# Kernel tuning notes

Hardware: AMD Instinct MI355X
Metric: run time of the kernel (lower is better)

## Reference

```python
import jax, jax.numpy as jnp
import numpy as np
from jax import lax

LEVEL = 128  # level_num

def _bn(x, g, b, m, v):
    # inference-mode BatchNorm, channel axis = 1
    sh = (1, -1) + (1,) * (x.ndim - 2)
    return (x - m.reshape(sh)) * (g.reshape(sh) * lax.rsqrt(v.reshape(sh) + 1e-5)) + b.reshape(sh)

def _leaky(a):
    return jnp.where(a > 0, a, 0.01 * a)

def _l2n(a):
    return a / jnp.maximum(jnp.linalg.norm(a, axis=1, keepdims=True), 1e-12)

def _resize_bilinear_ac(x, oh, ow):
    # bilinear, align_corners=True, NCHW
    n, c, h, w = x.shape
    ys = jnp.linspace(0.0, h - 1.0, oh)
    xs = jnp.linspace(0.0, w - 1.0, ow)
    y0 = jnp.floor(ys).astype(jnp.int32)
    x0 = jnp.floor(xs).astype(jnp.int32)
    y1 = jnp.minimum(y0 + 1, h - 1)
    x1 = jnp.minimum(x0 + 1, w - 1)
    wy = (ys - y0)[:, None]
    wx = (xs - x0)[None, :]
    Y0, Y1, X0, X1 = y0[:, None], y1[:, None], x0[None, :], x1[None, :]
    return (x[:, :, Y0, X0] * (1 - wy) * (1 - wx) + x[:, :, Y0, X1] * (1 - wy) * wx
            + x[:, :, Y1, X0] * wy * (1 - wx) + x[:, :, Y1, X1] * wy * wx)

def _forward(x, conv1_w, bn1_g, bn1_b, bn1_m, bn1_v, conv2_w, f1_w, f2_w, f2_g, f2_b, f2_m, f2_v,
             out1_w, out1_g, out1_b, out1_m, out1_v, k_w, q_w, v_w, out_w, out_g, out_b, out_m, out_v):
    # conv1: 3x3 conv + BN + LeakyReLU
    y = lax.conv_general_dilated(x, conv1_w, (1, 1), 'SAME', dimension_numbers=('NCHW', 'OIHW', 'NCHW'))
    y = _leaky(_bn(y, bn1_g, bn1_b, bn1_m, bn1_v))
    # conv2: 1x1 conv, 256->128
    x2 = jnp.einsum('nchw,oc->nohw', y, conv2_w)
    N, C, H, W = x2.shape  # C = 128
    x_ave = x2.mean(axis=(2, 3), keepdims=True)  # [N,C,1,1]
    cos = (_l2n(x_ave) * _l2n(x2)).sum(1)        # [N,H,W]
    sh, sw = H // 3, W // 3
    L = sh * sw
    # H,W divisible by 3 -> adaptive_avg_pool2d is identity
    cs = cos.reshape(N, 3, sh, 3, sw).transpose(0, 1, 3, 2, 4).reshape(N, 9, L).transpose(0, 2, 1)  # [N,L,9]
    # LBP bit packing vs center (index 4); weight 0 at index 4 (strict > gives 0 there)
    bits = (cs > cs[:, :, 4:5]).astype(x.dtype)
    wts = jnp.array([1, 2, 4, 8, 0, 16, 32, 64, 128], dtype=x.dtype)
    code = (bits * wts).sum(-1)  # [N,L]
    mn = code.min(-1, keepdims=True)
    mx = code.max(-1, keepdims=True)
    code = (code - mn) / (mx - mn)
    cmin = code.min(-1, keepdims=True)
    cmax = code.max(-1, keepdims=True)
    qlv = (2 * jnp.arange(LEVEL, dtype=x.dtype) + 1) / (2 * LEVEL) * (cmax - cmin) + cmin  # [N,LEVEL]
    inter = (qlv[:, 1] - qlv[:, 0])[:, None, None]  # [N,1,1]
    quant = 1 - jnp.abs(qlv[:, None, :] - code[:, :, None])  # [N,L,LEVEL]
    quant = jnp.where(quant > 1 - inter, quant, 0.0)
    sta = quant.sum(1)                                       # [N,LEVEL]
    sta = sta / sta.sum(-1, keepdims=True)
    sta2 = jnp.stack([qlv, sta], axis=1)                     # [N,2,LEVEL]
    h1 = _leaky(jnp.einsum('ncl,oc->nol', sta2, f1_w))       # f1: 2->64
    h2 = jax.nn.relu(_bn(jnp.einsum('ncl,oc->nol', h1, f2_w), f2_g, f2_b, f2_m, f2_v))  # f2: 64->128
    xa = jnp.broadcast_to(x_ave[:, :, 0, 0][:, :, None], (N, C, LEVEL))
    s = jnp.concatenate([h2, xa], axis=1)                    # [N,256,LEVEL]
    s = jax.nn.relu(_bn(jnp.einsum('ncl,oc->nol', s, out1_w), out1_g, out1_b, out1_m, out1_v))
    k = jnp.einsum('ncl,oc->nol', s, k_w)
    q = jnp.einsum('ncl,oc->nol', s, q_w)
    v = jnp.einsum('ncl,oc->nol', s, v_w)
    w = jax.nn.softmax(jnp.einsum('ncl,ncm->nlm', k, q), axis=-1)  # bmm(k^T, q)
    f = jnp.einsum('nlm,ncm->ncl', w, v)                            # bmm(w, v^T) then transpose
    f = jax.nn.relu(_bn(jnp.einsum('ncl,oc->nol', f, out_w), out_g, out_b, out_m, out_v))
    out = jnp.einsum('ncl,npl->ncp', f, quant).reshape(N, 256, sh, sh)  # bmm(f, quant^T)
    return _resize_bilinear_ac(out, H, W)

def setup_inputs() -> dict:
    key = jax.random.key(0)
    ks = jax.random.split(key, 16)
    f32 = jnp.float32
    def nrm(k, shape, s=0.05):
        return s * jax.random.normal(k, shape, f32)
    def bnp(k, c):
        k1, k2, k3, k4 = jax.random.split(k, 4)
        return (1.0 + 0.1 * jax.random.normal(k1, (c,), f32),
                0.1 * jax.random.normal(k2, (c,), f32),
                0.1 * jax.random.normal(k3, (c,), f32),
                jax.random.uniform(k4, (c,), f32, 0.5, 1.5))
    d = {}
    d['x'] = jax.random.normal(ks[0], (32, 512, 48, 48), f32)
    d['conv1_w'] = nrm(ks[1], (256, 512, 3, 3))
    d['bn1_g'], d['bn1_b'], d['bn1_m'], d['bn1_v'] = bnp(ks[2], 256)
    d['conv2_w'] = nrm(ks[3], (128, 256))
    d['f1_w'] = nrm(ks[4], (64, 2), 0.3)
    d['f2_w'] = nrm(ks[5], (128, 64), 0.1)
    d['f2_g'], d['f2_b'], d['f2_m'], d['f2_v'] = bnp(ks[6], 128)
    d['out1_w'] = nrm(ks[7], (256, 256))
    d['out1_g'], d['out1_b'], d['out1_m'], d['out1_v'] = bnp(ks[8], 256)
    d['k_w'] = nrm(ks[9], (256, 256))
    d['q_w'] = nrm(ks[10], (256, 256))
    d['v_w'] = nrm(ks[11], (256, 256))
    d['out_w'] = nrm(ks[12], (256, 256))
    d['out_g'], d['out_b'], d['out_m'], d['out_v'] = bnp(ks[13], 256)
    return d

def reference(x, conv1_w, bn1_g, bn1_b, bn1_m, bn1_v, conv2_w, f1_w, f2_w, f2_g, f2_b, f2_m, f2_v,
              out1_w, out1_g, out1_b, out1_m, out1_v, k_w, q_w, v_w, out_w, out_g, out_b, out_m, out_v):
    return _forward(x, conv1_w, bn1_g, bn1_b, bn1_m, bn1_v, conv2_w, f1_w, f2_w, f2_g, f2_b, f2_m, f2_v,
                    out1_w, out1_g, out1_b, out1_m, out1_v, k_w, q_w, v_w, out_w, out_g, out_b, out_m, out_v)
```

## Files before the change

### kernel.cpp

```cpp
#include <hip/hip_runtime.h>
#include <math.h>

#define N_IMG 32
#define P2304 2304
#define CIN 512
#define CMID 256
#define C2 128
#define LEV 128

typedef _Float16 half8 __attribute__((ext_vector_type(8)));
typedef float f32x16 __attribute__((ext_vector_type(16)));
typedef unsigned short u16;
typedef unsigned int u32;

__device__ __forceinline__ float wredSum(float v){
#pragma unroll
  for (int o = 32; o > 0; o >>= 1) v += __shfl_down(v, o, 64);
  return v;
}
__device__ __forceinline__ float wredMax(float v){
#pragma unroll
  for (int o = 32; o > 0; o >>= 1) v = fmaxf(v, __shfl_down(v, o, 64));
  return v;
}
// ... 35 lines not shown
__global__ void prep_w2_kernel(const float* __restrict__ w2,
                               uint4* __restrict__ Wh, uint4* __restrict__ Wl){
  int fid = blockIdx.x * 256 + threadIdx.x;
  int lam = fid & 63;
  int c32 = (fid >> 6) & 3;
  int kt  = fid >> 8;
  int co = c32 * 32 + (lam & 31);
  half8 vh, vl;
#pragma unroll
  for (int j = 0; j < 8; ++j){
    int k = kt * 16 + ((lam >> 5) << 3) + j;
    float v = w2[co * CMID + k];
    _Float16 h = (_Float16)v;
    vh[j] = h;
    vl[j] = (_Float16)((v - (float)h) * 2048.0f);
  }
  Wh[fid] = *(uint4*)&vh;
  Wl[fid] = *(uint4*)&vl;
}

__global__ void prep_bn_kernel(const float* __restrict__ g1, const float* __restrict__ b1,
                               const float* __restrict__ m1, const float* __restrict__ v1,
                               float* __restrict__ s1, float* __restrict__ t1){
  int c = threadIdx.x;
  float s = g1[c] * (1.0f / sqrtf(v1[c] + 1e-5f));
  s1[c] = s;
  t1[c] = b1[c] - m1[c] * s;
}

__global__ void prep_x_kernel(const float* __restrict__ x,
                              u16* __restrict__ xh, u16* __restrict__ xl,
                              int n0){
  __shared__ float tile[128 * 49];
  const int t = threadIdx.x;
  const int b = blockIdx.x;
  const int n_loc = b / 50;
  const int hp = b - n_loc * 50;
  const int n = n0 + n_loc;
  const int h = hp - 1;
  const bool vrow = (h >= 0) && (h < 48);
  const size_t base_n = (size_t)n_loc * 1280000;
  for (int cc = 0; cc < 4; ++cc){
    if (vrow){
      const float* src = x + (((size_t)n * 512 + cc * 128) * 48 + h) * 48;
#pragma unroll
      for (int i = 0; i < 24; ++i){
        int idx = t + 256 * i;
        int w = idx % 48;
        int c = idx / 48;
        tile[c * 49 + w] = src[(size_t)c * 2304 + w];
      }
    }
    __syncthreads();
    for (int i = 0; i < 13; ++i){
      int idx = t + 256 * i;
      if (idx < 3200){
        int ck_loc = idx / 400;
        int rem = idx - ck_loc * 400;
        int wp = rem >> 3;
        int clp = rem & 7;
        int w = wp - 1;
        int c_loc = ck_loc * 16 + clp * 2;
        float v0 = 0.f, v1 = 0.f;
        if (vrow && (unsigned)w < 48u){
          v0 = tile[c_loc * 49 + w];
          v1 = tile[(c_loc + 1) * 49 + w];
        }
        _Float16 h0 = (_Float16)v0, h1 = (_Float16)v1;
        _Float16 l0 = (_Float16)((v0 - (float)h0) * 2048.0f);
        _Float16 l1 = (_Float16)((v1 - (float)h1) * 2048.0f);
        union { _Float16 hh[2]; u32 uu; } ph, pl;
        ph.hh[0] = h0; ph.hh[1] = h1;
        pl.hh[0] = l0; pl.hh[1] = l1;
        size_t off = base_n + ((size_t)(cc * 8 + ck_loc) * 2500
                               + hp * 50 + wp) * 16 + clp * 2;
        *(u32*)(xh + off) = ph.uu;
        *(u32*)(xl + off) = pl.uu;
      }
    }
    __syncthreads();
  }
}

#define COMPUTE_M(CUR, KF)                                                    \
  {                                                                           \
    const int ct0 = (g & 1) * 2, pt0 = (g >> 1) * 2;                          \
    half8 fAh[2], fAl[2], fBh[2], fBl[2];                                     \
    _Pragma("unroll")                                                         \
    for (int a = 0; a < 2; ++a){                                              \
      fAh[a] = *(half8*)&Abuf[CUR][KF][0][(ct0 + a) * 512 + lam * 8];         \
      fAl[a] = *(half8*)&Abuf[CUR][KF][1][(ct0 + a) * 512 + lam * 8];         \
      fBh[a] = *(half8*)&Bbuf[CUR][KF][0][(pt0 + a) * 512 + lam * 8];         \
      fBl[a] = *(half8*)&Bbuf[CUR][KF][1][(pt0 + a) * 512 + lam * 8];         \
    }                                                                         \
    _Pragma("unroll")                                                         \
    for (int a = 0; a < 2; ++a)                                               \
      _Pragma("unroll")                                                       \
      for (int b = 0; b < 2; ++b){                                            \
        acc_hh[a][b] = __builtin_amdgcn_mfma_f32_32x32x16_f16(                \
            fAh[a], fBh[b], acc_hh[a][b], 0, 0, 0);                           \
        acc_x[a][b] = __builtin_amdgcn_mfma_f32_32x32x16_f16(                 \
            fAh[a], fBl[b], acc_x[a][b], 0, 0, 0);                            \
        acc_x[a][b] = __builtin_amdgcn_mfma_f32_32x32x16_f16(                 \
            fAl[a], fBh[b], acc_x[a][b], 0, 0, 0);                            \
      }                                                                       \
  }

#define WAITV8  asm volatile("s_waitcnt vmcnt(8)"  ::: "memory")
#define WAITV0  asm volatile("s_waitcnt vmcnt(0)"  ::: "memory")
#define BARSB { __builtin_amdgcn_s_barrier(); __builtin_amdgcn_sched_barrier(0); }

template<int NC>
__global__ __launch_bounds__(256, 2) void conv1_lds_kernel(
    const u16* __restrict__ xh, const u16* __restrict__ xl,
    const uint4* __restrict__ Wh, const uint4* __restrict__ Wl,
    const float* __restrict__ s1, const float* __restrict__ t1,
    u16* __restrict__ yh, u16* __restrict__ yl, int n0)
{
  __shared__ _Float16 Abuf[2][2][2][2048];
  __shared__ _Float16 Bbuf[2][2][2][2048];
  const int t = threadIdx.x;
  const int lam = t & 63;
  const int g = t >> 6;

  const int xcd = blockIdx.x & 7;
  const int rest = blockIdx.x >> 3;
  const int NPX = NC / 8;
  const int n_loc = xcd * NPX + rest / 36;
  const int inner = rest % 36;
  const int pt_blk = inner % 18;
  const int cot = inner / 18;
  const int n = n0 + n_loc;

  const int pbase = pt_blk * 128;
  const int khi = lam >> 5;
  const int pp = (g << 5) + (lam & 31);
  const int p = pbase + pp;
  const int ph = p / 48, pw = p - ph * 48;
  const u16* xh_n = xh + (size_t)n_loc * 1280000;
  const u16* xl_n = xl + (size_t)n_loc * 1280000;

  const int S = 144;

  f32x16 acc_hh[2][2], acc_x[2][2];
#pragma unroll
  for (int a = 0; a < 2; ++a)
#pragma unroll
    for (int b = 0; b < 2; ++b){
#pragma unroll
      for (int e = 0; e < 16; ++e){ acc_hh[a][b][e] = 0.f; acc_x[a][b][e] = 0.f; }
    }

#define ISSUE1(SV, BUF)                                                       \
  {                                                                           \
    int s_ = (SV);                                                            \
    int k0_ = 2 * s_;                                                         \
    _Pragma("unroll")                                                         \
    for (int kf = 0; kf < 2; ++kf){                                           \
      int fg_ = ((k0_ + kf) * 2 + cot) * 4 + g;                               \
      gll16(Wh + fg_ * 64 + lam, &Abuf[BUF][kf][0][t * 8]);                   \
      gll16(Wl + fg_ * 64 + lam, &Abuf[BUF][kf][1][t * 8]);                   \
    }                                                                         \
    int r_ = k0_ >> 5;                                          \
    int ck0_ = k0_ & 31;                         \
    int qpp_ = (ph + r_ / 3) * 50 + (pw + r_ % 3);            \
    _Pragma("unroll")                                                         \
    for (int kf = 0; kf < 2; ++kf){                                           \
      size_t o_ = ((size_t)(ck0_ + kf) * 2500 + qpp_) * 16 + (khi << 3);      \
      gll16(xh_n + o_, &Bbuf[BUF][kf][0][t * 8]);                             \
      gll16(xl_n + o_, &Bbuf[BUF][kf][1][t * 8]);                             \
    }                                                                         \
  }

  ISSUE1(0, 0);
  ISSUE1(1, 1);

  for (int s = 0; s < S - 1; ++s){
    WAITV8;
    BARSB;
    __builtin_amdgcn_s_setprio(1);
    COMPUTE_M(s & 1, 0);
    COMPUTE_M(s & 1, 1);
    __builtin_amdgcn_s_setprio(0);
    if (s + 2 < S){
      BARSB;
      ISSUE1(s + 2, s & 1);
    }
  }
  WAITV0;
  BARSB;
  __builtin_amdgcn_s_setprio(1);
  COMPUTE_M((S - 1) & 1, 0);
  COMPUTE_M((S - 1) & 1, 1);
  __builtin_amdgcn_s_setprio(0);
#undef ISSUE1

  const int cobase = cot * 128;
#pragma unroll
  for (int a = 0; a < 2; ++a){
    const int ctile = (g & 1) * 2 + a;
#pragma unroll
    for (int b = 0; b < 2; ++b){
      const int ptile = (g >> 1) * 2 + b;
      const int pg = pbase + ptile * 32 + (lam & 31);
#pragma unroll
      for (int q = 0; q < 4; ++q){
        const int co0 = cobase + ctile * 32 + 8 * q + 4 * khi;
        const int co16 = co0 >> 4, col = co0 & 15;
        union { _Float16 h[4]; uint2 u; } Uh, Ul;
#pragma unroll
        for (int i = 0; i < 4; ++i){
          const int rg = 4 * q + i;
          const int co = co0 + i;
          float val = acc_hh[a][b][rg] + acc_x[a][b][rg] * (1.0f / 2048.0f);
          val = val * s1[co] + t1[co];
          val = val > 0.f ? val : 0.01f * val;
          _Float16 h = (_Float16)val;
          Uh.h[i] = h;
          Ul.h[i] = (_Float16)((val - (float)h) * 2048.0f);
        }
        size_t off = (((size_t)n * 16 + co16) * P2304 + pg) * 16 + col;
        *(uint2*)(yh + off) = Uh.u;
        *(uint2*)(yl + off) = Ul.u;
      }
    }
  }
}

__global__ __launch_bounds__(256, 2) void conv2_lds_kernel(
    const u16* __restrict__ yh, const u16* __restrict__ yl,
    const uint4* __restrict__ Wh, const uint4* __restrict__ Wl,
    float* __restrict__ out)
{
  __shared__ _Float16 Abuf[2][2][2][2048];
  __shared__ _Float16 Bbuf[2][2][2][2048];
  const int t = threadIdx.x;
  const int lam = t & 63;
  const int g = t >> 6;

  const int pt_blk = blockIdx.x % 18;
  const int n = blockIdx.x / 18;
  const int pbase = pt_blk * 128;
  const int khi = lam >> 5;
  const int p = pbase + (g << 5) + (lam & 31);
  const u16* yh_n = yh + (size_t)n * 589824;
  const u16* yl_n = yl + (size_t)n * 589824;

  const int S = 8;

  f32x16 acc_hh[2][2], acc_x[2][2];
#pragma unroll
  for (int a = 0; a < 2; ++a)
#pragma unroll
    for (int b = 0; b < 2; ++b){
#pragma unroll
      for (int e = 0; e < 16; ++e){ acc_hh[a][b][e] = 0.f; acc_x[a][b][e] = 0.f; }
    }

#define ISSUE2(SV, BUF)                                                       \
  {                                                                           \
    int s_ = (SV);                                                            \
    int k0_ = 2 * s_;                                                         \
    _Pragma("unroll")                                                         \
    for (int kf = 0; kf < 2; ++kf){                                           \
      int fg_ = (k0_ + kf) * 4 + g;                                           \
      gll16(Wh + fg_ * 64 + lam, &Abuf[BUF][kf][0][t * 8]);                   \
      gll16(Wl + fg_ * 64 + lam, &Abuf[BUF][kf][1][t * 8]);                   \
    }                                                                         \
    _Pragma("unroll")                                                         \
    for (int kf = 0; kf < 2; ++kf){                                           \
      size_t o_ = ((size_t)(k0_ + kf) * P2304 + p) * 16 + (khi << 3);         \
      gll16(yh_n + o_, &Bbuf[BUF][kf][0][t * 8]);                             \
      gll16(yl_n + o_, &Bbuf[BUF][kf][1][t * 8]);                             \
    }                                                                         \
  }

  ISSUE2(0, 0);
  ISSUE2(1, 1);

  for (int s = 0; s < S - 1; ++s){
    WAITV8;
    BARSB;
    __builtin_amdgcn_s_setprio(1);
    COMPUTE_M(s & 1, 0);
    COMPUTE_M(s & 1, 1);
    __builtin_amdgcn_s_setprio(0);
    if (s + 2 < S){
      BARSB;
      ISSUE2(s + 2, s & 1);
    }
  }
  WAITV0;
  BARSB;
  __builtin_amdgcn_s_setprio(1);
  COMPUTE_M((S - 1) & 1, 0);
  COMPUTE_M((S - 1) & 1, 1);
  __builtin_amdgcn_s_setprio(0);
#undef ISSUE2

#pragma unroll
  for (int a = 0; a < 2; ++a){
    const int ctile = (g & 1) * 2 + a;
#pragma unroll
    for (int b = 0; b < 2; ++b){
      const int ptile = (g >> 1) * 2 + b;
      const int pg = pbase + ptile * 32 + (lam & 31);
#pragma unroll
      for (int rg = 0; rg < 16; ++rg){
        const int row = (rg & 3) + 8 * (rg >> 2) + 4 * khi;
        const int co = ctile * 32 + row;
        float val = acc_hh[a][b][rg] + acc_x[a][b][rg] * (1.0f / 2048.0f);
        out[((size_t)n * C2 + co) * P2304 + pg] = val;
      }
    }
  }
}

template<int R, int CPT, int COTN, bool BN>
__global__ __launch_bounds__(256, 2) void conv_mfma_kernel(
    const float* __restrict__ in, const uint4* __restrict__ Wh, const uint4* __restrict__ Wl,
    const float* __restrict__ s1, const float* __restrict__ t1, float* __restrict__ out)
{
  __shared__ _Float16 Abuf[2][2][2][2048];
  __shared__ _Float16 Bbuf[2][2][2][2048];
  const int t = threadIdx.x;
  const int lam = t & 63;
  const int g = t >> 6;

  int n, pt_blk, cot;
  if (COTN == 2){
    int xcd = blockIdx.x & 7;
    int rest = blockIdx.x >> 3;
    n = xcd * 4 + rest / 36;
    int inner = rest % 36;
    pt_blk = inner % 18;
    cot = inner / 18;
  } else {
    pt_blk = blockIdx.x % 18;
    cot = 0;
    n = blockIdx.x / 18;
  }
  const int pbase = pt_blk * 128;
  const int cobase = cot * 128;

  const int khi = lam >> 5;
  const int pp = (g << 5) + (lam & 31);
  const int p = pbase + pp;
  const int ph = p / 48, pw = p - ph * 48;
  const float* in_n = in + (size_t)n * CPT * P2304;

  const int S = (R * CPT) / 32;
  const int KTPT = CPT / 16;

  f32x16 acc_hh[2][2], acc_x[2][2];
#pragma unroll
  for (int a = 0; a < 2; ++a)
#pragma unroll
    for (int b = 0; b < 2; ++b){
#pragma unroll
      for (int e = 0; e < 16; ++e){ acc_hh[a][b][e] = 0.f; acc_x[a][b][e] = 0.f; }
    }

  uint4 rAh[2], rAl[2];
  float rB[16];
  bool vmask;

#define ISSUE(SV)                                                             \
  {                                                                           \
    int s_ = (SV);                                                            \
    _Pragma("unroll")                                                         \
    for (int kf = 0; kf < 2; ++kf){                                           \
      int fi = (((2 * s_ + kf) * COTN + cot) * 4 + g) * 64 + lam;             \
      rAh[kf] = Wh[fi];                                                       \
      rAl[kf] = Wl[fi];                                                       \
    }                                                                         \
    int r_ = (R == 1) ? 0 : ((2 * s_) / KTPT);                                \
    int cbase_ = ((2 * s_) % KTPT) * 16;                                      \
    int dh_ = (R == 1) ? 0 : (r_ / 3 - 1);                                    \
    int dw_ = (R == 1) ? 0 : (r_ - (r_ / 3) * 3 - 1);                         \
    int hh_ = ph + dh_, ww_ = pw + dw_;                                       \
    vmask = ((unsigned)hh_ < 48u) & ((unsigned)ww_ < 48u);                    \
    int hc_ = min(max(hh_, 0), 47), wc_ = min(max(ww_, 0), 47);               \
    const float* src_ = in_n + hc_ * 48 + wc_                                 \
                        + (size_t)(cbase_ + khi * 8) * P2304;                 \
    _Pragma("unroll")                                                         \
    for (int kf = 0; kf < 2; ++kf)                                            \
      _Pragma("unroll")                                                       \
      for (int j = 0; j < 8; ++j)                                             \
        rB[kf * 8 + j] = src_[(kf * 16 + j) * P2304];                         \
  }

#define STASH(NXT)                                                            \
  {                                                                           \
    _Pragma("unroll")                                                         \
    for (int kf = 0; kf < 2; ++kf){                                           \
      *(uint4*)&Abuf[NXT][kf][0][t * 8] = rAh[kf];                            \
      *(uint4*)&Abuf[NXT][kf][1][t * 8] = rAl[kf];                            \
      half8 vh, vl;                                                           \
      _Pragma("unroll")                                                       \
      for (int j = 0; j < 8; ++j){                                            \
        float v = vmask ? rB[kf * 8 + j] : 0.0f;                              \
        _Float16 h = (_Float16)v;                                             \
        vh[j] = h;                                                            \
        vl[j] = (_Float16)((v - (float)h) * 2048.0f);                         \
      }                                                                       \
      *(half8*)&Bbuf[NXT][kf][0][t * 8] = vh;                                 \
      *(half8*)&Bbuf[NXT][kf][1][t * 8] = vl;                                 \
    }                                                                         \
  }

  ISSUE(0);
  STASH(0);
  __syncthreads();

  for (int s = 0; s < S; ++s){
    const int cur = s & 1, nxt = cur ^ 1;
    const bool more = (s + 1 < S);
    if (more) ISSUE(s + 1);
    COMPUTE_M(cur, 0);
    if (more) STASH(nxt);
    COMPUTE_M(cur, 1);
    __syncthreads();
  }
#undef ISSUE
#undef STASH

  const int M = COTN * 128;
#pragma unroll
  for (int a = 0; a < 2; ++a){
    const int ctile = (g & 1) * 2 + a;
#pragma unroll
    for (int b = 0; b < 2; ++b){
      const int ptile = (g >> 1) * 2 + b;
      const int pg = pbase + ptile * 32 + (lam & 31);
#pragma unroll
      for (int rg = 0; rg < 16; ++rg){
        const int row = (rg & 3) + 8 * (rg >> 2) + 4 * (lam >> 5);
        const int co = cobase + ctile * 32 + row;
        float val = acc_hh[a][b][rg] + acc_x[a][b][rg] * (1.0f / 2048.0f);
        if (BN){
          val = val * s1[co] + t1[co];
          val = val > 0.f ? val : 0.01f * val;
        }
        out[((size_t)n * M + co) * P2304 + pg] = val;
      }
    }
  }
}

__global__ void xave_kernel(const float* __restrict__ x2, float* __restrict__ xave){
  __shared__ float red[4];
  int nc = blockIdx.x, t = threadIdx.x;
  const float* row = x2 + nc * P2304;
  float s = 0.f;
#pragma unroll
  for (int i = 0; i < 9; i++) s += row[t + 256 * i];
  float w = wredSum(s);
  if ((t & 63) == 0) red[t >> 6] = w;
  __syncthreads();
  if (t == 0) xave[nc] = (red[0] + red[1] + red[2] + red[3]) * (1.0f / 2304.0f);
}

__global__ void xan_kernel(const float* __restrict__ xave, float* __restrict__ xan){
  __shared__ float red[2];
  int n = blockIdx.x, t = threadIdx.x;
  float v = xave[n * 128 + t];
  float w = wredSum(v * v);
  if ((t & 63) == 0) red[t >> 6] = w;
  __syncthreads();
  float norm = fmaxf(sqrtf(red[0] + red[1]), 1e-12f);
  xan[n * 128 + t] = v / norm;
}

__global__ void cos_kernel(const float* __restrict__ x2, const float* __restrict__ xan,
                           float* __restrict__ cosb){
  int idx = blockIdx.x * 256 + threadIdx.x;
  if (idx >= N_IMG * P2304) return;
  int n = idx / P2304;
  int p = idx - n * P2304;
  const float* xp = x2 + n * C2 * P2304 + p;
  const float* an = xan + n * 128;
  float dot = 0.f, ss = 0.f;
  for (int c = 0; c < 128; c++){
    float v = xp[c * P2304];
    dot += an[c] * v;
    ss  += v * v;
  }
  cosb[idx] = dot / fmaxf(sqrtf(ss), 1e-12f);
}

__global__ void lbp_kernel(const float* __restrict__ cosb, float* __restrict__ code,
                           float* __restrict__ qlv){
  __shared__ float red[4];
  int n = blockIdx.x;
  int l = threadIdx.x;
  int ir = l >> 4, ic = l & 15;
  const float* cn = cosb + n * P2304;
  float cs4 = cn[(16 + ir) * 48 + (16 + ic)];
  const float wts[9] = {1.f, 2.f, 4.f, 8.f, 0.f, 16.f, 32.f, 64.f, 128.f};
  float codev = 0.f;
#pragma unroll
  for (int j = 0; j < 9; j++){
    int jr = j / 3, jc = j - 3 * (j / 3);
    float vv = cn[(jr * 16 + ir) * 48 + (jc * 16 + ic)];
    if (vv > cs4) codev += wts[j];
  }
  float w;
  w = wredMin(codev);
  if ((l & 63) == 0) red[l >> 6] = w;
  __syncthreads();
  float mn = fminf(fminf(red[0], red[1]), fminf(red[2], red[3]));
  __syncthreads();
  w = wredMax(codev);
  if ((l & 63) == 0) red[l >> 6] = w;
  __syncthreads();
  float mx = fmaxf(fmaxf(red[0], red[1]), fmaxf(red[2], red[3]));
  __syncthreads();
  float cd = (codev - mn) / (mx - mn);
  w = wredMin(cd);
  if ((l & 63) == 0) red[l >> 6] = w;
  __syncthreads();
  float cmin = fminf(fminf(red[0], red[1]), fminf(red[2], red[3]));
  __syncthreads();
  w = wredMax(cd);
  if ((l & 63) == 0) red[l >> 6] = w;
  __syncthreads();
  float cmax = fmaxf(fmaxf(red[0], red[1]), fmaxf(red[2], red[3]));
  code[n * 256 + l] = cd;
  if (l < 128){
    float tmp = (float)(2 * l + 1) * (1.0f / 256.0f);
    qlv[n * 128 + l] = tmp * (cmax - cmin) + cmin;
  }
}

__global__ void quant_kernel(const float* __restrict__ code, const float* __restrict__ qlv,
                             float* __restrict__ quantT){
  __shared__ float cs[256];
  __shared__ float qs[128];
  int n = blockIdx.x, t = threadIdx.x;
  cs[t] = code[n * 256 + t];
  if (t < 128) qs[t] = qlv[n * 128 + t];
  __syncthreads();
  float thr = 1.0f - (qs[1] - qs[0]);
  float* dst = quantT + n * LEV * 256;
#pragma unroll 4
  for (int i = 0; i < 128; i++){
    int v = t + 256 * i;
    int lv = v >> 8;
    int p = v & 255;
    float qq = 1.0f - fabsf(qs[lv] - cs[p]);
    dst[v] = (qq > thr) ? qq : 0.f;
  }
}

__global__ void sta_kernel(const float* __restrict__ quantT, float* __restrict__ sta){
  __shared__ float red[2];
  int n = blockIdx.x, i = threadIdx.x;
  const float* qr = quantT + (n * LEV + i) * 256;
  float s = 0.f;
  for (int p = 0; p < 256; p++) s += qr[p];
  float w = wredSum(s);
  if ((i & 63) == 0) red[i >> 6] = w;
  __syncthreads();
  float tot = red[0] + red[1];
  sta[n * 128 + i] = s / tot;
}

__global__ void h1_kernel(const float* __restrict__ f1w, const float* __restrict__ qlv,
                          const float* __restrict__ sta, float* __restrict__ h1){
  int idx = blockIdx.x * 256 + threadIdx.x;
  if (idx >= N_IMG * 64 * 128) return;
  int l = idx & 127;
  int n = idx >> 13;
  int o = (idx >> 7) & 63;
  float a = f1w[o * 2] * qlv[n * 128 + l] + f1w[o * 2 + 1] * sta[n * 128 + l];
  h1[idx] = a > 0.f ? a : 0.01f * a;
}

__global__ void gemm_w_kernel(const float* __restrict__ Wm, const float* __restrict__ B,
                              float* __restrict__ Cout, int Cdim, int O, int total, int mode,
                              const float* __restrict__ g, const float* __restrict__ bb,
                              const float* __restrict__ mm, const float* __restrict__ vv){
  int idx = blockIdx.x * 256 + threadIdx.x;
  if (idx >= total) return;
  int per_n = (O >> 2) << 7;
  int n = idx / per_n;
  int rem = idx - n * per_n;
  int o0 = (rem >> 7) << 2;
  int l = rem & 127;
  const float* Bn = B + (n * Cdim) * 128 + l;
  const float* w0 = Wm + (o0 + 0) * Cdim;
  const float* w1 = Wm + (o0 + 1) * Cdim;
  const float* w2 = Wm + (o0 + 2) * Cdim;
  const float* w3 = Wm + (o0 + 3) * Cdim;
  float a0 = 0, a1 = 0, a2 = 0, a3 = 0;
  for (int c = 0; c < Cdim; c++){
    float bv = Bn[c * 128];
    a0 += w0[c] * bv; a1 += w1[c] * bv; a2 += w2[c] * bv; a3 += w3[c] * bv;
  }
  float av[4] = {a0, a1, a2, a3};
#pragma unroll
  for (int j = 0; j < 4; j++){
    int o = o0 + j;
    float val = av[j];
    if (mode == 1){
      float s = g[o] * (1.0f / sqrtf(vv[o] + 1e-5f));
      val = (val - mm[o]) * s + bb[o];
      val = fmaxf(val, 0.f);
    }
    Cout[(n * O + o) * 128 + l] = val;
  }
}

__global__ void concat_kernel(const float* __restrict__ h2, const float* __restrict__ xave,
                              float* __restrict__ s){
  int idx = blockIdx.x * 256 + threadIdx.x;
  if (idx >= N_IMG * 256 * 128) return;
  int l = idx & 127;
  int c = (idx >> 7) & 255;
  int n = idx >> 15;
  s[idx] = (c < 128) ? h2[(n * 128 + c) * 128 + l] : xave[n * 128 + (c - 128)];
}

__global__ void attn_sc_kernel(const float* __restrict__ k, const float* __restrict__ q,
                               float* __restrict__ sc){
  int idx = blockIdx.x * 256 + threadIdx.x;
  if (idx >= N_IMG * 32 * 128) return;
  int m = idx & 127;
  int l0 = ((idx >> 7) & 31) << 2;
  int n = idx >> 12;
  const float* kn = k + n * 256 * 128;
  const float* qn = q + n * 256 * 128 + m;
  float a0 = 0, a1 = 0, a2 = 0, a3 = 0;
  for (int c = 0; c < 256; c++){
    float qv = qn[c * 128];
    const float* kr = kn + c * 128 + l0;
    a0 += kr[0] * qv; a1 += kr[1] * qv; a2 += kr[2] * qv; a3 += kr[3] * qv;
  }
  float* dst = sc + (n * 128 + l0) * 128 + m;
  dst[0] = a0; dst[128] = a1; dst[256] = a2; dst[384] = a3;
}

__global__ void softmax_kernel(float* __restrict__ sc){
  __shared__ float red[2];
  int row = blockIdx.x;
  int t = threadIdx.x;
  float v = sc[row * 128 + t];
  float w = wredMax(v);
  if ((t & 63) == 0) red[t >> 6] = w;
  __syncthreads();
  float mx = fmaxf(red[0], red[1]);
  float e = expf(v - mx);
  float s = wredSum(e);
  __syncthreads();
  if ((t & 63) == 0) red[t >> 6] = s;
  __syncthreads();
  sc[row * 128 + t] = e / (red[0] + red[1]);
}

__global__ void transpose_sc_kernel(const float* __restrict__ sc, float* __restrict__ scT){
  int idx = blockIdx.x * 256 + threadIdx.x;
  if (idx >= N_IMG * 128 * 128) return;
  int l = idx & 127;
  int m = (idx >> 7) & 127;
  int n = idx >> 14;
  scT[idx] = sc[(n * 128 + l) * 128 + m];
}

__global__ void attn_f_kernel(const float* __restrict__ vb, const float* __restrict__ scT,
                              float* __restrict__ f){
  int idx = blockIdx.x * 256 + threadIdx.x;
  if (idx >= N_IMG * 64 * 128) return;
  int l = idx & 127;
  int c0 = ((idx >> 7) & 63) << 2;
  int n = idx >> 13;
  const float* vn = vb + (n * 256 + c0) * 128;
  const float* sn = scT + n * 128 * 128 + l;
  float a0 = 0, a1 = 0, a2 = 0, a3 = 0;
  for (int m = 0; m < 128; m++){
    float sv = sn[m * 128];
    a0 += vn[m] * sv; a1 += vn[128 + m] * sv; a2 += vn[256 + m] * sv; a3 += vn[384 + m] * sv;
  }
  float* dst = f + (n * 256 + c0) * 128 + l;
  dst[0] = a0; dst[128] = a1; dst[256] = a2; dst[384] = a3;
}

__global__ void final_kernel(const float* __restrict__ g, const float* __restrict__ quantT,
                             float* __restrict__ outs){
  int idx = blockIdx.x * 256 + threadIdx.x;
  if (idx >= N_IMG * 64 * 256) return;
  int p = idx & 255;
  int c0 = ((idx >> 8) & 63) << 2;
  int n = idx >> 14;
  const float* gn = g + (n * 256 + c0) * 128;
// ... 10 lines not shown
__global__ void resize_kernel(const float* __restrict__ outs, float* __restrict__ dout){
  int idx = blockIdx.x * 256 + threadIdx.x;
  if (idx >= N_IMG * 256 * P2304) return;
  int ow = idx % 48;
  int tmp = idx / 48;
  int oh = tmp % 48;
  int nc = tmp / 48;
  const float* src = outs + nc * 256;
  float fy = oh * (15.0f / 47.0f);
  float fx = ow * (15.0f / 47.0f);
  int y0 = (int)fy;
  int x0 = (int)fx;
  int y1 = min(y0 + 1, 15);
  int x1 = min(x0 + 1, 15);
  float wy = fy - (float)y0;
  float wx = fx - (float)x0;
  float v00 = src[y0 * 16 + x0], v01 = src[y0 * 16 + x1];
  float v10 = src[y1 * 16 + x0], v11 = src[y1 * 16 + x1];
  dout[idx] = v00 * (1.f - wy) * (1.f - wx) + v01 * (1.f - wy) * wx
            + v10 * wy * (1.f - wx) + v11 * wy * wx;
}

extern "C" void kernel_launch(void* const* d_in, const int* in_sizes, int n_in,
                              void* d_out, int out_size, void* d_ws, size_t ws_size,
                              hipStream_t stream)
{
  const float* x       = (const float*)d_in[0];
  const float* conv1_w = (const float*)d_in[1];
  const float* bn1_g   = (const float*)d_in[2];
  const float* bn1_b   = (const float*)d_in[3];
  const float* bn1_m   = (const float*)d_in[4];
  const float* bn1_v   = (const float*)d_in[5];
  const float* conv2_w = (const float*)d_in[6];
  const float* f1_w    = (const float*)d_in[7];
  const float* f2_w    = (const float*)d_in[8];
  const float* f2_g    = (const float*)d_in[9];
  const float* f2_b    = (const float*)d_in[10];
  const float* f2_m    = (const float*)d_in[11];
  const float* f2_v    = (const float*)d_in[12];
  const float* out1_w  = (const float*)d_in[13];
  const float* out1_g  = (const float*)d_in[14];
  const float* out1_b  = (const float*)d_in[15];
  const float* out1_m  = (const float*)d_in[16];
  const float* out1_v  = (const float*)d_in[17];
  const float* k_w     = (const float*)d_in[18];
  const float* q_w     = (const float*)d_in[19];
  const float* v_w     = (const float*)d_in[20];
  const float* out_w   = (const float*)d_in[21];
  const float* out_g   = (const float*)d_in[22];
  const float* out_b   = (const float*)d_in[23];
  const float* out_m   = (const float*)d_in[24];
  const float* out_v   = (const float*)d_in[25];

  float* ws = (float*)d_ws;
  float* dout = (float*)d_out;

  float* w_y   = ws;
  float* w_x2  = ws + 18874368;
  float* w_W1h = ws + 28311552;
  float* w_W1l = ws + 28901376;
  float* w_W2h = ws + 29491200;
  float* w_W2l = ws + 29507584;
  float* w_s1  = ws + 29523968;
  float* w_t1  = ws + 29524224;
  float* w_xave = w_y + 0;
  float* w_xan  = w_y + 4096;
  float* w_cos  = w_y + 8192;
  float* w_code = w_y + 81920;
  float* w_qlv  = w_y + 90112;
  float* w_sta  = w_y + 94208;
  float* w_quant= w_y + 98304;
  float* w_h1   = w_y + 1146880;
  float* w_h2   = w_y + 1409024;
  float* w_s    = w_y + 1933312;
  float* w_k    = w_y + 2981888;
  float* w_q    = w_y + 4030464;
  float* w_v    = w_y + 5079040;
  float* w_sc   = w_y + 6127616;
  float* w_scT  = w_y + 6651904;
  float* w_f    = w_y + 7176192;
  float* w_g    = w_y + 8224768;
  float* w_outs = w_y + 9273344;
  float* w_s2   = w_y + 11370496;

  prep_w1_kernel<<<576, 256, 0, stream>>>(conv1_w, (uint4*)w_W1h, (uint4*)w_W1l);
  prep_w2_kernel<<<16, 256, 0, stream>>>(conv2_w, (uint4*)w_W2h, (uint4*)w_W2l);
  prep_bn_kernel<<<1, 256, 0, stream>>>(bn1_g, bn1_b, bn1_m, bn1_v, w_s1, w_t1);

  const size_t BASE_F = 29524480;
  const size_t XPI_F  = 640000;
  const size_t ws_f = ws_size / 4;
  int NCc = 0;
  if (ws_f >= BASE_F + 2 * 32 * XPI_F)      NCc = 32;
  else if (ws_f >= BASE_F + 2 * 16 * XPI_F) NCc = 16;

  if (NCc > 0){
    u16* w_xh = (u16*)(ws + BASE_F);
    u16* w_xl = w_xh + (size_t)NCc * 1280000;
    u16* w_yh = (u16*)w_y;
    u16* w_yl = (u16*)(w_y + 9437184);
    const int nchunk = N_IMG / NCc;
    for (int c = 0; c < nchunk; ++c){
      int n0 = c * NCc;
      prep_x_kernel<<<NCc * 50, 256, 0, stream>>>(x, w_xh, w_xl, n0);
      if (NCc == 32)
        conv1_lds_kernel<32><<<1152, 256, 0, stream>>>(
            w_xh, w_xl, (const uint4*)w_W1h, (const uint4*)w_W1l, w_s1, w_t1,
            w_yh, w_yl, n0);
      else
        conv1_lds_kernel<16><<<576, 256, 0, stream>>>(
            w_xh, w_xl, (const uint4*)w_W1h, (const uint4*)w_W1l, w_s1, w_t1,
            w_yh, w_yl, n0);
    }
    conv2_lds_kernel<<<576, 256, 0, stream>>>(
        w_yh, w_yl, (const uint4*)w_W2h, (const uint4*)w_W2l, w_x2);
  } else {
    conv_mfma_kernel<9, 512, 2, true><<<1152, 256, 0, stream>>>(
        x, (const uint4*)w_W1h, (const uint4*)w_W1l, w_s1, w_t1, w_y);
    conv_mfma_kernel<1, 256, 1, false><<<576, 256, 0, stream>>>(
        w_y, (const uint4*)w_W2h, (const uint4*)w_W2l, w_s1, w_t1, w_x2);
  }

  xave_kernel<<<4096, 256, 0, stream>>>(w_x2, w_xave);
  xan_kernel<<<32, 128, 0, stream>>>(w_xave, w_xan);
  cos_kernel<<<288, 256, 0, stream>>>(w_x2, w_xan, w_cos);
  lbp_kernel<<<32, 256, 0, stream>>>(w_cos, w_code, w_qlv);
  quant_kernel<<<32, 256, 0, stream>>>(w_code, w_qlv, w_quant);
  sta_kernel<<<32, 128, 0, stream>>>(w_quant, w_sta);
  h1_kernel<<<1024, 256, 0, stream>>>(f1_w, w_qlv, w_sta, w_h1);
  gemm_w_kernel<<<512, 256, 0, stream>>>(f2_w, w_h1, w_h2, 64, 128, N_IMG * 32 * 128, 1,
                                         f2_g, f2_b, f2_m, f2_v);
  concat_kernel<<<4096, 256, 0, stream>>>(w_h2, w_xave, w_s);
  gemm_w_kernel<<<1024, 256, 0, stream>>>(out1_w, w_s, w_s2, 256, 256, N_IMG * 64 * 128, 1,
                                          out1_g, out1_b, out1_m, out1_v);
  gemm_w_kernel<<<1024, 256, 0, stream>>>(k_w, w_s2, w_k, 256, 256, N_IMG * 64 * 128, 0,
                                          nullptr, nullptr, nullptr, nullptr);
  gemm_w_kernel<<<1024, 256, 0, stream>>>(q_w, w_s2, w_q, 256, 256, N_IMG * 64 * 128, 0,
                                          nullptr, nullptr, nullptr, nullptr);
  gemm_w_kernel<<<1024, 256, 0, stream>>>(v_w, w_s2, w_v, 256, 256, N_IMG * 64 * 128, 0,
                                          nullptr, nullptr, nullptr, nullptr);
  attn_sc_kernel<<<512, 256, 0, stream>>>(w_k, w_q, w_sc);
  softmax_kernel<<<4096, 128, 0, stream>>>(w_sc);
  transpose_sc_kernel<<<2048, 256, 0, stream>>>(w_sc, w_scT);
  attn_f_kernel<<<1024, 256, 0, stream>>>(w_v, w_scT, w_f);
  gemm_w_kernel<<<1024, 256, 0, stream>>>(out_w, w_f, w_g, 256, 256, N_IMG * 64 * 128, 1,
                                          out_g, out_b, out_m, out_v);
  final_kernel<<<2048, 256, 0, stream>>>(w_g, w_quant, w_outs);
  resize_kernel<<<73728, 256, 0, stream>>>(w_outs, dout);
}
```

Baseline: 1.624 ms.

## Deepen conv pipelines to 4 stages, split sta reduction, fuse k/q/v GEMMs

The conv1 and conv2 LDS kernels move from double-buffered two-k-fragment stages to a four-buffer ring with one k-fragment per stage and three loads in flight. This drops the second barrier per iteration and is meant to hide global-load latency better. The sta reduction is split into a wide row-sum kernel plus a small normalize kernel to raise parallelism. The three k/q/v weight GEMMs are merged into one launch. The trade-off is more barriers per unit of work, since stages are now half as large, plus one extra launch for sta.

```diff
diff --git a/kernel.cpp b/kernel.cpp
--- a/kernel.cpp
+++ b/kernel.cpp
@@ -141,7 +141,214 @@
   }
 }
 
-#define COMPUTE_M(CUR, KF)                                                    \
+#define COMPUTE_R(CUR)                                                        \
+  {                                                                           \
+    const int ct0 = (g & 1) * 2, pt0 = (g >> 1) * 2;                          \
+    half8 fAh[2], fAl[2], fBh[2], fBl[2];                                     \
+    _Pragma("unroll")                                                         \
+    for (int a = 0; a < 2; ++a){                                              \
+      fAh[a] = *(half8*)&Abuf[CUR][0][(ct0 + a) * 512 + lam * 8];             \
+      fAl[a] = *(half8*)&Abuf[CUR][1][(ct0 + a) * 512 + lam * 8];             \
+      fBh[a] = *(half8*)&Bbuf[CUR][0][(pt0 + a) * 512 + lam * 8];             \
+      fBl[a] = *(half8*)&Bbuf[CUR][1][(pt0 + a) * 512 + lam * 8];             \
+    }                                                                         \
+    _Pragma("unroll")                                                         \
+    for (int a = 0; a < 2; ++a)                                               \
+      _Pragma("unroll")                                                       \
+      for (int b = 0; b < 2; ++b){                                            \
+        acc_hh[a][b] = __builtin_amdgcn_mfma_f32_32x32x16_f16(                \
+            fAh[a], fBh[b], acc_hh[a][b], 0, 0, 0);                           \
+        acc_x[a][b] = __builtin_amdgcn_mfma_f32_32x32x16_f16(                 \
+            fAh[a], fBl[b], acc_x[a][b], 0, 0, 0);                            \
+        acc_x[a][b] = __builtin_amdgcn_mfma_f32_32x32x16_f16(                 \
+            fAl[a], fBh[b], acc_x[a][b], 0, 0, 0);                            \
+      }                                                                       \
+  }
+
+#define WAITV8  asm volatile("s_waitcnt vmcnt(8)"  ::: "memory")
+#define WAITV4  asm volatile("s_waitcnt vmcnt(4)"  ::: "memory")
+#define WAITV0  asm volatile("s_waitcnt vmcnt(0)"  ::: "memory")
+#define BARSB { __builtin_amdgcn_s_barrier(); __builtin_amdgcn_sched_barrier(0); }
+
+template<int NC>
+__global__ __launch_bounds__(256, 2) void conv1_lds_kernel(
+    const u16* __restrict__ xh, const u16* __restrict__ xl,
+    const uint4* __restrict__ Wh, const uint4* __restrict__ Wl,
+    const float* __restrict__ s1, const float* __restrict__ t1,
+    u16* __restrict__ yh, u16* __restrict__ yl, int n0)
+{
+  __shared__ _Float16 Abuf[4][2][2048];
+  __shared__ _Float16 Bbuf[4][2][2048];
+  const int t = threadIdx.x;
+  const int lam = t & 63;
+  const int g = t >> 6;
+
+  const int xcd = blockIdx.x & 7;
+  const int rest = blockIdx.x >> 3;
+  const int NPX = NC / 8;
+  const int n_loc = xcd * NPX + rest / 36;
+  const int inner = rest % 36;
+  const int pt_blk = inner % 18;
+  const int cot = inner / 18;
+  const int n = n0 + n_loc;
+
+  const int pbase = pt_blk * 128;
+  const int khi = lam >> 5;
+  const int pp = (g << 5) + (lam & 31);
+  const int p = pbase + pp;
+  const int ph = p / 48, pw = p - ph * 48;
+  const u16* xh_n = xh + (size_t)n_loc * 1280000;
+  const u16* xl_n = xl + (size_t)n_loc * 1280000;
+
+  const int S = 288;
+
+  f32x16 acc_hh[2][2], acc_x[2][2];
+#pragma unroll
+  for (int a = 0; a < 2; ++a)
+#pragma unroll
+    for (int b = 0; b < 2; ++b){
+#pragma unroll
+      for (int e = 0; e < 16; ++e){ acc_hh[a][b][e] = 0.f; acc_x[a][b][e] = 0.f; }
+    }
+
+#define ISSUE1(SV, BUF)                                                       \
+  {                                                                           \
+    int s_ = (SV);                                                            \
+    int fg_ = (s_ * 2 + cot) * 4 + g;                                         \
+    gll16(Wh + fg_ * 64 + lam, &Abuf[BUF][0][t * 8]);                         \
+    gll16(Wl + fg_ * 64 + lam, &Abuf[BUF][1][t * 8]);                         \
+    int r_ = s_ >> 5;                                           \
+    int ck_ = s_ & 31;                                       \
+    int qpp_ = (ph + r_ / 3) * 50 + (pw + r_ % 3);            \
+    size_t o_ = ((size_t)ck_ * 2500 + qpp_) * 16 + (khi << 3);                \
+    gll16(xh_n + o_, &Bbuf[BUF][0][t * 8]);                                   \
+    gll16(xl_n + o_, &Bbuf[BUF][1][t * 8]);                                   \
+  }
+
+  ISSUE1(0, 0);
+  ISSUE1(1, 1);
+  ISSUE1(2, 2);
+
+  for (int s = 0; s < S; ++s){
+    if (s < S - 2)      { WAITV8; }
+    else if (s == S - 2){ WAITV4; }
+    else                { WAITV0; }
+    BARSB;
+    __builtin_amdgcn_s_setprio(1);
+    COMPUTE_R(s & 3);
+    __builtin_amdgcn_s_setprio(0);
+    if (s + 3 < S) ISSUE1(s + 3, (s + 3) & 3);
+  }
+#undef ISSUE1
+
+  const int cobase = cot * 128;
+#pragma unroll
+  for (int a = 0; a < 2; ++a){
+    const int ctile = (g & 1) * 2 + a;
+#pragma unroll
+    for (int b = 0; b < 2; ++b){
+      const int ptile = (g >> 1) * 2 + b;
+      const int pg = pbase + ptile * 32 + (lam & 31);
+#pragma unroll
+      for (int q = 0; q < 4; ++q){
+        const int co0 = cobase + ctile * 32 + 8 * q + 4 * khi;
+        const int co16 = co0 >> 4, col = co0 & 15;
+        union { _Float16 h[4]; uint2 u; } Uh, Ul;
+#pragma unroll
+        for (int i = 0; i < 4; ++i){
+          const int rg = 4 * q + i;
+          const int co = co0 + i;
+          float val = acc_hh[a][b][rg] + acc_x[a][b][rg] * (1.0f / 2048.0f);
+          val = val * s1[co] + t1[co];
+          val = val > 0.f ? val : 0.01f * val;
+          _Float16 h = (_Float16)val;
+          Uh.h[i] = h;
+          Ul.h[i] = (_Float16)((val - (float)h) * 2048.0f);
+        }
+        size_t off = (((size_t)n * 16 + co16) * P2304 + pg) * 16 + col;
+        *(uint2*)(yh + off) = Uh.u;
+        *(uint2*)(yl + off) = Ul.u;
+      }
+    }
+  }
+}
+
+__global__ __launch_bounds__(256, 2) void conv2_lds_kernel(
+    const u16* __restrict__ yh, const u16* __restrict__ yl,
+    const uint4* __restrict__ Wh, const uint4* __restrict__ Wl,
+    float* __restrict__ out)
+{
+  __shared__ _Float16 Abuf[4][2][2048];
+  __shared__ _Float16 Bbuf[4][2][2048];
+  const int t = threadIdx.x;
+  const int lam = t & 63;
+  const int g = t >> 6;
+
+  const int pt_blk = blockIdx.x % 18;
+  const int n = blockIdx.x / 18;
+  const int pbase = pt_blk * 128;
+  const int khi = lam >> 5;
+  const int p = pbase + (g << 5) + (lam & 31);
+  const u16* yh_n = yh + (size_t)n * 589824;
+  const u16* yl_n = yl + (size_t)n * 589824;
+
+  const int S = 16;
+
+  f32x16 acc_hh[2][2], acc_x[2][2];
+#pragma unroll
+  for (int a = 0; a < 2; ++a)
+#pragma unroll
+    for (int b = 0; b < 2; ++b){
+#pragma unroll
+      for (int e = 0; e < 16; ++e){ acc_hh[a][b][e] = 0.f; acc_x[a][b][e] = 0.f; }
+    }
+
+#define ISSUE2(SV, BUF)                                                       \
+  {                                                                           \
+    int s_ = (SV);                                                            \
+    int fg_ = s_ * 4 + g;                                                     \
+    gll16(Wh + fg_ * 64 + lam, &Abuf[BUF][0][t * 8]);                         \
+    gll16(Wl + fg_ * 64 + lam, &Abuf[BUF][1][t * 8]);                         \
+    size_t o_ = ((size_t)s_ * P2304 + p) * 16 + (khi << 3);                   \
+    gll16(yh_n + o_, &Bbuf[BUF][0][t * 8]);                                   \
+    gll16(yl_n + o_, &Bbuf[BUF][1][t * 8]);                                   \
+  }
+
+  ISSUE2(0, 0);
+  ISSUE2(1, 1);
+  ISSUE2(2, 2);
+
+  for (int s = 0; s < S; ++s){
+    if (s < S - 2)      { WAITV8; }
+    else if (s == S - 2){ WAITV4; }
+    else                { WAITV0; }
+    BARSB;
+    __builtin_amdgcn_s_setprio(1);
+    COMPUTE_R(s & 3);
+    __builtin_amdgcn_s_setprio(0);
+    if (s + 3 < S) ISSUE2(s + 3, (s + 3) & 3);
+  }
+#undef ISSUE2
+
+#pragma unroll
+  for (int a = 0; a < 2; ++a){
+    const int ctile = (g & 1) * 2 + a;
+#pragma unroll
+    for (int b = 0; b < 2; ++b){
+      const int ptile = (g >> 1) * 2 + b;
+      const int pg = pbase + ptile * 32 + (lam & 31);
+#pragma unroll
+      for (int rg = 0; rg < 16; ++rg){
+        const int row = (rg & 3) + 8 * (rg >> 2) + 4 * khi;
+        const int co = ctile * 32 + row;
+        float val = acc_hh[a][b][rg] + acc_x[a][b][rg] * (1.0f / 2048.0f);
+        out[((size_t)n * C2 + co) * P2304 + pg] = val;
+      }
+    }
+  }
+}
+
+#define COMPUTE_F(CUR, KF)                                                    \
   {                                                                           \
     const int ct0 = (g & 1) * 2, pt0 = (g >> 1) * 2;                          \
     half8 fAh[2], fAl[2], fBh[2], fBl[2];                                     \
@@ -164,216 +371,6 @@
             fAl[a], fBh[b], acc_x[a][b], 0, 0, 0);                            \
       }                                                                       \
   }
-
-#define WAITV8  asm volatile("s_waitcnt vmcnt(8)"  ::: "memory")
-#define WAITV0  asm volatile("s_waitcnt vmcnt(0)"  ::: "memory")
-#define BARSB { __builtin_amdgcn_s_barrier(); __builtin_amdgcn_sched_barrier(0); }
-
-template<int NC>
-__global__ __launch_bounds__(256, 2) void conv1_lds_kernel(
-    const u16* __restrict__ xh, const u16* __restrict__ xl,
-    const uint4* __restrict__ Wh, const uint4* __restrict__ Wl,
-    const float* __restrict__ s1, const float* __restrict__ t1,
-    u16* __restrict__ yh, u16* __restrict__ yl, int n0)
-{
-  __shared__ _Float16 Abuf[2][2][2][2048];
-  __shared__ _Float16 Bbuf[2][2][2][2048];
-  const int t = threadIdx.x;
-  const int lam = t & 63;
-  const int g = t >> 6;
-
-  const int xcd = blockIdx.x & 7;
-  const int rest = blockIdx.x >> 3;
-  const int NPX = NC / 8;
-  const int n_loc = xcd * NPX + rest / 36;
-  const int inner = rest % 36;
-  const int pt_blk = inner % 18;
-  const int cot = inner / 18;
-  const int n = n0 + n_loc;
-
-  const int pbase = pt_blk * 128;
-  const int khi = lam >> 5;
-  const int pp = (g << 5) + (lam & 31);
-  const int p = pbase + pp;
-  const int ph = p / 48, pw = p - ph * 48;
-  const u16* xh_n = xh + (size_t)n_loc * 1280000;
-  const u16* xl_n = xl + (size_t)n_loc * 1280000;
-
-  const int S = 144;
-
-  f32x16 acc_hh[2][2], acc_x[2][2];
-#pragma unroll
-  for (int a = 0; a < 2; ++a)
-#pragma unroll
-    for (int b = 0; b < 2; ++b){
-#pragma unroll
-      for (int e = 0; e < 16; ++e){ acc_hh[a][b][e] = 0.f; acc_x[a][b][e] = 0.f; }
-    }
-
-#define ISSUE1(SV, BUF)                                                       \
-  {                                                                           \
-    int s_ = (SV);                                                            \
-    int k0_ = 2 * s_;                                                         \
-    _Pragma("unroll")                                                         \
-    for (int kf = 0; kf < 2; ++kf){                                           \
-      int fg_ = ((k0_ + kf) * 2 + cot) * 4 + g;                               \
-      gll16(Wh + fg_ * 64 + lam, &Abuf[BUF][kf][0][t * 8]);                   \
-      gll16(Wl + fg_ * 64 + lam, &Abuf[BUF][kf][1][t * 8]);                   \
-    }                                                                         \
-    int r_ = k0_ >> 5;                                          \
-    int ck0_ = k0_ & 31;                         \
-    int qpp_ = (ph + r_ / 3) * 50 + (pw + r_ % 3);            \
-    _Pragma("unroll")                                                         \
-    for (int kf = 0; kf < 2; ++kf){                                           \
-      size_t o_ = ((size_t)(ck0_ + kf) * 2500 + qpp_) * 16 + (khi << 3);      \
-      gll16(xh_n + o_, &Bbuf[BUF][kf][0][t * 8]);                             \
-      gll16(xl_n + o_, &Bbuf[BUF][kf][1][t * 8]);                             \
-    }                                                                         \
-  }
-
-  ISSUE1(0, 0);
-  ISSUE1(1, 1);
-
-  for (int s = 0; s < S - 1; ++s){
-    WAITV8;
-    BARSB;
-    __builtin_amdgcn_s_setprio(1);
-    COMPUTE_M(s & 1, 0);
-    COMPUTE_M(s & 1, 1);
-    __builtin_amdgcn_s_setprio(0);
-    if (s + 2 < S){
-      BARSB;
-      ISSUE1(s + 2, s & 1);
-    }
-  }
-  WAITV0;
-  BARSB;
-  __builtin_amdgcn_s_setprio(1);
-  COMPUTE_M((S - 1) & 1, 0);
-  COMPUTE_M((S - 1) & 1, 1);
-  __builtin_amdgcn_s_setprio(0);
-#undef ISSUE1
-
-  const int cobase = cot * 128;
-#pragma unroll
-  for (int a = 0; a < 2; ++a){
-    const int ctile = (g & 1) * 2 + a;
-#pragma unroll
-    for (int b = 0; b < 2; ++b){
-      const int ptile = (g >> 1) * 2 + b;
-      const int pg = pbase + ptile * 32 + (lam & 31);
-#pragma unroll
-      for (int q = 0; q < 4; ++q){
-        const int co0 = cobase + ctile * 32 + 8 * q + 4 * khi;
-        const int co16 = co0 >> 4, col = co0 & 15;
-        union { _Float16 h[4]; uint2 u; } Uh, Ul;
-#pragma unroll
-        for (int i = 0; i < 4; ++i){
-          const int rg = 4 * q + i;
-          const int co = co0 + i;
-          float val = acc_hh[a][b][rg] + acc_x[a][b][rg] * (1.0f / 2048.0f);
-          val = val * s1[co] + t1[co];
-          val = val > 0.f ? val : 0.01f * val;
-          _Float16 h = (_Float16)val;
-          Uh.h[i] = h;
-          Ul.h[i] = (_Float16)((val - (float)h) * 2048.0f);
-        }
-        size_t off = (((size_t)n * 16 + co16) * P2304 + pg) * 16 + col;
-        *(uint2*)(yh + off) = Uh.u;
-        *(uint2*)(yl + off) = Ul.u;
-      }
-    }
-  }
-}
-
-__global__ __launch_bounds__(256, 2) void conv2_lds_kernel(
-    const u16* __restrict__ yh, const u16* __restrict__ yl,
-    const uint4* __restrict__ Wh, const uint4* __restrict__ Wl,
-    float* __restrict__ out)
-{
-  __shared__ _Float16 Abuf[2][2][2][2048];
-  __shared__ _Float16 Bbuf[2][2][2][2048];
-  const int t = threadIdx.x;
-  const int lam = t & 63;
-  const int g = t >> 6;
-
-  const int pt_blk = blockIdx.x % 18;
-  const int n = blockIdx.x / 18;
-  const int pbase = pt_blk * 128;
-  const int khi = lam >> 5;
-  const int p = pbase + (g << 5) + (lam & 31);
-  const u16* yh_n = yh + (size_t)n * 589824;
-  const u16* yl_n = yl + (size_t)n * 589824;
-
-  const int S = 8;
-
-  f32x16 acc_hh[2][2], acc_x[2][2];
-#pragma unroll
-  for (int a = 0; a < 2; ++a)
-#pragma unroll
-    for (int b = 0; b < 2; ++b){
-#pragma unroll
-      for (int e = 0; e < 16; ++e){ acc_hh[a][b][e] = 0.f; acc_x[a][b][e] = 0.f; }
-    }
-
-#define ISSUE2(SV, BUF)                                                       \
-  {                                                                           \
-    int s_ = (SV);                                                            \
-    int k0_ = 2 * s_;                                                         \
-    _Pragma("unroll")                                                         \
-    for (int kf = 0; kf < 2; ++kf){                                           \
-      int fg_ = (k0_ + kf) * 4 + g;                                           \
-      gll16(Wh + fg_ * 64 + lam, &Abuf[BUF][kf][0][t * 8]);                   \
-      gll16(Wl + fg_ * 64 + lam, &Abuf[BUF][kf][1][t * 8]);                   \
-    }                                                                         \
-    _Pragma("unroll")                                                         \
-    for (int kf = 0; kf < 2; ++kf){                                           \
-      size_t o_ = ((size_t)(k0_ + kf) * P2304 + p) * 16 + (khi << 3);         \
-      gll16(yh_n + o_, &Bbuf[BUF][kf][0][t * 8]);                             \
-      gll16(yl_n + o_, &Bbuf[BUF][kf][1][t * 8]);                             \
-    }                                                                         \
-  }
-
-  ISSUE2(0, 0);
-  ISSUE2(1, 1);
-
-  for (int s = 0; s < S - 1; ++s){
-    WAITV8;
-    BARSB;
-    __builtin_amdgcn_s_setprio(1);
-    COMPUTE_M(s & 1, 0);
-    COMPUTE_M(s & 1, 1);
-    __builtin_amdgcn_s_setprio(0);
-    if (s + 2 < S){
-      BARSB;
-      ISSUE2(s + 2, s & 1);
-    }
-  }
-  WAITV0;
-  BARSB;
-  __builtin_amdgcn_s_setprio(1);
-  COMPUTE_M((S - 1) & 1, 0);
-  COMPUTE_M((S - 1) & 1, 1);
-  __builtin_amdgcn_s_setprio(0);
-#undef ISSUE2
-
-#pragma unroll
-  for (int a = 0; a < 2; ++a){
-    const int ctile = (g & 1) * 2 + a;
-#pragma unroll
-    for (int b = 0; b < 2; ++b){
-      const int ptile = (g >> 1) * 2 + b;
-      const int pg = pbase + ptile * 32 + (lam & 31);
-#pragma unroll
-      for (int rg = 0; rg < 16; ++rg){
-        const int row = (rg & 3) + 8 * (rg >> 2) + 4 * khi;
-        const int co = ctile * 32 + row;
-        float val = acc_hh[a][b][rg] + acc_x[a][b][rg] * (1.0f / 2048.0f);
-        out[((size_t)n * C2 + co) * P2304 + pg] = val;
-      }
-    }
-  }
-}
 
 template<int R, int CPT, int COTN, bool BN>
 __global__ __launch_bounds__(256, 2) void conv_mfma_kernel(
@@ -476,9 +473,9 @@
     const int cur = s & 1, nxt = cur ^ 1;
     const bool more = (s + 1 < S);
     if (more) ISSUE(s + 1);
-    COMPUTE_M(cur, 0);
+    COMPUTE_F(cur, 0);
     if (more) STASH(nxt);
-    COMPUTE_M(cur, 1);
+    COMPUTE_F(cur, 1);
     __syncthreads();
   }
 #undef ISSUE
@@ -612,17 +609,27 @@
   }
 }
 
-__global__ void sta_kernel(const float* __restrict__ quantT, float* __restrict__ sta){
+__global__ void sta_rows_kernel(const float* __restrict__ quantT, float* __restrict__ raw){
+  int b = blockIdx.x;
+  int t = threadIdx.x;
+  int n = b >> 5;
+  int row = (b & 31) * 4 + (t >> 6);
+  int lane = t & 63;
+  const float* src = quantT + ((size_t)(n * LEV + row)) * 256 + lane * 4;
+  float4 v = *(const float4*)src;
+  float s = v.x + v.y + v.z + v.w;
+  s = wredSum(s);
+  if (lane == 0) raw[n * 128 + row] = s;
+}
+
+__global__ void sta_norm_kernel(const float* __restrict__ raw, float* __restrict__ sta){
   __shared__ float red[2];
-  int n = blockIdx.x, i = threadIdx.x;
-  const float* qr = quantT + (n * LEV + i) * 256;
-  float s = 0.f;
-  for (int p = 0; p < 256; p++) s += qr[p];
-  float w = wredSum(s);
-  if ((i & 63) == 0) red[i >> 6] = w;
-  __syncthreads();
-  float tot = red[0] + red[1];
-  sta[n * 128 + i] = s / tot;
+  int n = blockIdx.x, t = threadIdx.x;
+  float v = raw[n * 128 + t];
+  float w = wredSum(v);
+  if ((t & 63) == 0) red[t >> 6] = w;
+  __syncthreads();
+  sta[n * 128 + t] = v / (red[0] + red[1]);
 }
 
 __global__ void h1_kernel(const float* __restrict__ f1w, const float* __restrict__ qlv,
@@ -669,6 +676,33 @@
     }
     Cout[(n * O + o) * 128 + l] = val;
   }
+}
+
+__global__ void gemm_kqv_kernel(const float* __restrict__ kW, const float* __restrict__ qW,
+                                const float* __restrict__ vW, const float* __restrict__ B,
+                                float* __restrict__ kO, float* __restrict__ qO,
+                                float* __restrict__ vO){
+  int idx = blockIdx.x * 256 + threadIdx.x;
+  int sel = idx >> 18;
+  int rem = idx & 262143;
+  const float* Wm = (sel == 0) ? kW : (sel == 1) ? qW : vW;
+  float* Cout     = (sel == 0) ? kO : (sel == 1) ? qO : vO;
+  int n = rem >> 13;
+  int r2 = rem & 8191;
+  int o0 = (r2 >> 7) << 2;
+  int l = r2 & 127;
+  const float* Bn = B + (n * 256) * 128 + l;
+  const float* w0 = Wm + (o0 + 0) * 256;
+  const float* w1 = Wm + (o0 + 1) * 256;
+  const float* w2 = Wm + (o0 + 2) * 256;
+  const float* w3 = Wm + (o0 + 3) * 256;
+  float a0 = 0, a1 = 0, a2 = 0, a3 = 0;
+  for (int c = 0; c < 256; c++){
+    float bv = Bn[c * 128];
+    a0 += w0[c] * bv; a1 += w1[c] * bv; a2 += w2[c] * bv; a3 += w3[c] * bv;
+  }
+  float* dst = Cout + (n * 256 + o0) * 128 + l;
+  dst[0] = a0; dst[128] = a1; dst[256] = a2; dst[384] = a3;
 }
 
 __global__ void concat_kernel(const float* __restrict__ h2, const float* __restrict__ xave,
@@ -845,6 +879,7 @@
   float* w_g    = w_y + 8224768;
   float* w_outs = w_y + 9273344;
   float* w_s2   = w_y + 11370496;
+  float* w_raw  = w_y + 12419072;
 
   prep_w1_kernel<<<576, 256, 0, stream>>>(conv1_w, (uint4*)w_W1h, (uint4*)w_W1l);
   prep_w2_kernel<<<16, 256, 0, stream>>>(conv2_w, (uint4*)w_W2h, (uint4*)w_W2l);
@@ -889,19 +924,15 @@
   cos_kernel<<<288, 256, 0, stream>>>(w_x2, w_xan, w_cos);
   lbp_kernel<<<32, 256, 0, stream>>>(w_cos, w_code, w_qlv);
   quant_kernel<<<32, 256, 0, stream>>>(w_code, w_qlv, w_quant);
-  sta_kernel<<<32, 128, 0, stream>>>(w_quant, w_sta);
+  sta_rows_kernel<<<1024, 256, 0, stream>>>(w_quant, w_raw);
+  sta_norm_kernel<<<32, 128, 0, stream>>>(w_raw, w_sta);
   h1_kernel<<<1024, 256, 0, stream>>>(f1_w, w_qlv, w_sta, w_h1);
   gemm_w_kernel<<<512, 256, 0, stream>>>(f2_w, w_h1, w_h2, 64, 128, N_IMG * 32 * 128, 1,
                                          f2_g, f2_b, f2_m, f2_v);
   concat_kernel<<<4096, 256, 0, stream>>>(w_h2, w_xave, w_s);
   gemm_w_kernel<<<1024, 256, 0, stream>>>(out1_w, w_s, w_s2, 256, 256, N_IMG * 64 * 128, 1,
                                           out1_g, out1_b, out1_m, out1_v);
-  gemm_w_kernel<<<1024, 256, 0, stream>>>(k_w, w_s2, w_k, 256, 256, N_IMG * 64 * 128, 0,
-                                          nullptr, nullptr, nullptr, nullptr);
-  gemm_w_kernel<<<1024, 256, 0, stream>>>(q_w, w_s2, w_q, 256, 256, N_IMG * 64 * 128, 0,
-                                          nullptr, nullptr, nullptr, nullptr);
-  gemm_w_kernel<<<1024, 256, 0, stream>>>(v_w, w_s2, w_v, 256, 256, N_IMG * 64 * 128, 0,
-                                          nullptr, nullptr, nullptr, nullptr);
+  gemm_kqv_kernel<<<3072, 256, 0, stream>>>(k_w, q_w, v_w, w_s2, w_k, w_q, w_v);
   attn_sc_kernel<<<512, 256, 0, stream>>>(w_k, w_q, w_sc);
   softmax_kernel<<<4096, 128, 0, stream>>>(w_sc);
   transpose_sc_kernel<<<2048, 256, 0, stream>>>(w_sc, w_scT);
```

Measured after the change: 1.623 ms. No clear change (-0.1%).
